# Optimization experiments

Measured on AMD Instinct MI355X. Metric: run time of the kernel, lower is better.

## Reference

```python
import math
import jax, jax.numpy as jnp
import numpy as np

# ---- module hyperparams (from init_kwargs defaults) ----
NUM_AA, EMB_DIM, K, EXCLUDE = 20, 16, 64, 2
R_ON, R_CUT, DELTA, WALL = 8.0, 10.0, 0.3, 10.0
RHO_MIN, RHO_MAX, RHO_BASE = 1.6, 2.8, 2.0
B, L = 8, 2048
BIG = 1e9  # masks excluded pairs in the distance matrix


def setup_inputs() -> dict:
    key = jax.random.key(0)
    k1, k2, k3 = jax.random.split(key, 3)
    # coordinates scaled to a realistic Angstrom spread so switch/softplus are exercised
    R = jax.random.normal(k1, (B, L, 3), dtype=jnp.float32) * 10.0
    seq = jax.random.randint(k2, (B, L), 0, NUM_AA, dtype=jnp.int64)
    # learned params: AA embedding table + size head (small random weight, bias at rho_base)
    emb_table = jax.random.normal(k3, (NUM_AA, EMB_DIM), dtype=jnp.float32)
    size_w = 0.1 * jax.random.normal(jax.random.fold_in(key, 7), (1, EMB_DIM), dtype=jnp.float32)
    frac = (RHO_BASE - RHO_MIN) / max(1e-6, RHO_MAX - RHO_MIN)
    frac = min(0.999, max(0.001, frac))
    size_b = jnp.full((1,), math.log(frac / (1.0 - frac)), dtype=jnp.float32)
    return {"R": R, "seq": seq, "emb_table": emb_table, "size_w": size_w, "size_b": size_b}


def _rho(s, emb_table, size_w, size_b):
    # per-residue learned radius in [RHO_MIN, RHO_MAX]; s: int indices, any shape
    e = emb_table[s]                                  # (..., EMB_DIM)
    x = jnp.einsum('...d,d->...', e, size_w[0]) + size_b[0]
    return RHO_MIN + (RHO_MAX - RHO_MIN) * jax.nn.sigmoid(x)


def _smooth_switch(r):
    # smoothstep from 1 (r<=R_ON) down to 0 (r>=R_CUT)
    t = jnp.clip((r - R_ON) / (R_CUT - R_ON), 0.0, 1.0)
    return 1.0 - t * t * (3.0 - 2.0 * t)


def reference(R, seq, emb_table, size_w, size_b):
    b, l, _ = R.shape
    # pairwise distances (B, L, L)
    diff = R[:, :, None, :] - R[:, None, :, :]
    D = jnp.sqrt(jnp.maximum(jnp.sum(diff * diff, axis=-1), 1e-12))
    # exclude bonded/near-diagonal pairs |i-j| <= EXCLUDE (includes self)
    idx = jnp.arange(l)
    excl = jnp.abs(idx[:, None] - idx[None, :]) <= EXCLUDE
    Dm = jnp.where(excl[None], BIG, D)
    # K smallest distances per residue -> negate for lax.top_k
    neg_r, j = jax.lax.top_k(-Dm, K)                  # (B, L, K)
    r = -neg_r
    # gather neighbor sequence ids along L
    seq_j = jnp.take_along_axis(jnp.broadcast_to(seq[:, :, None], (b, l, K)), j, axis=1)
    # pair radius r0_ij = rho(s_i) + rho(s_j)
    rho_i = _rho(seq, emb_table, size_w, size_b)[:, :, None]   # (B, L, 1)
    rho_j = _rho(seq_j, emb_table, size_w, size_b)             # (B, L, K)
    r0 = rho_i + rho_j
    rep = WALL * jax.nn.softplus((r0 - r) / (DELTA + 1e-12))
    return (rep * _smooth_switch(r)).sum(axis=(1, 2))          # (B,)
```

## Files before the change

### kernel.cpp

```cpp
#include <hip/hip_runtime.h>
#include <hip/hip_fp16.h>
#include <math.h>

#define LRES 2048
#define NB 8
#define KSEL 64
#define EMBD 16
#define NAA 20
#define NBIN 128
#define BINSCALE 1.28f
#define BINW 0.78125f

static __device__ __forceinline__ float fdot2u(unsigned a, unsigned b, float c) {
#if __has_builtin(__builtin_amdgcn_fdot2)
    typedef _Float16 h2f __attribute__((ext_vector_type(2)));
    union { unsigned u; h2f h; } ua, ub;
    ua.u = a; ub.u = b;
    return __builtin_amdgcn_fdot2(ua.h, ub.h, c, false);
#else
    float d;
    asm("v_dot2_f32_f16 %0, %1, %2, %3" : "=v"(d) : "v"(a), "v"(b), "v"(c));
    return d;
#endif
}

static __device__ __forceinline__ unsigned hadd2u(unsigned a, unsigned b) {
    __half2 ha = *(__half2*)&a, hb = *(__half2*)&b;
    __half2 r = __hadd2(ha, hb);
    return *(unsigned*)&r;
}

template <int CTRL, int RM>
static __device__ __forceinline__ unsigned dpp_u(unsigned v) {
    return (unsigned)__builtin_amdgcn_update_dpp(0, (int)v, CTRL, RM, 0xf, true);
}
static __device__ __forceinline__ unsigned wave_iscan_u(unsigned s) {
    s += dpp_u<0x111, 0xf>(s);
    s += dpp_u<0x112, 0xf>(s);
    s += dpp_u<0x114, 0xf>(s);
    s += dpp_u<0x118, 0xf>(s);
    s += dpp_u<0x142, 0xa>(s);
    s += dpp_u<0x143, 0xc>(s);
    return s;
}
static __device__ __forceinline__ float wave_iscan_f(float a) {
    a += __uint_as_float(dpp_u<0x111, 0xf>(__float_as_uint(a)));
    a += __uint_as_float(dpp_u<0x112, 0xf>(__float_as_uint(a)));
    a += __uint_as_float(dpp_u<0x114, 0xf>(__float_as_uint(a)));
    a += __uint_as_float(dpp_u<0x118, 0xf>(__float_as_uint(a)));
    a += __uint_as_float(dpp_u<0x142, 0xa>(__float_as_uint(a)));
    a += __uint_as_float(dpp_u<0x143, 0xc>(__float_as_uint(a)));
    return a;
}

#define LDS_FENCE() asm volatile("s_waitcnt lgkmcnt(0)" ::: "memory")

__global__ __launch_bounds__(512, 8) void repel_kernel(
    const float* __restrict__ R,
    const int* __restrict__ seq,
    const float* __restrict__ emb,
    const float* __restrict__ wv,
    const float* __restrict__ bias,
    float* __restrict__ partial)
{
    const int tid  = threadIdx.x;
    const int w    = tid >> 6;
    const int lane = tid & 63;
    const int row  = blockIdx.x * 8 + w;
    const int b    = row >> 11;
    const int i    = row & (LRES - 1);

    __shared__ uint2    Pl[LRES];
    __shared__ unsigned hist[8][NBIN];
    __shared__ float    rho_tab[NAA];
    __shared__ unsigned shT[8];
    __shared__ float    shS[8];

    const float* __restrict__ Rb = R + b * (LRES * 3);
    const int*   __restrict__ Sb = seq + b * LRES;

    if (tid < NAA) {
        float x = bias[0];
#pragma unroll
        for (int d = 0; d < EMBD; ++d) x += emb[tid * EMBD + d] * wv[d];
        rho_tab[tid] = 1.6f + 1.2f / (1.0f + __expf(-x));
    }
    __syncthreads();

#pragma unroll
    for (int q = 0; q < 4; ++q) {
        int p = (q << 9) + tid;
        float x = Rb[p * 3 + 0], y = Rb[p * 3 + 1], z = Rb[p * 3 + 2];
        float rho = rho_tab[Sb[p]];
        __half2 h0 = __floats2half2_rn(x, y);
        __half2 h1 = __floats2half2_rn(z, rho);
        Pl[p] = make_uint2(*(unsigned*)&h0, *(unsigned*)&h1);
    }

    *(uint2*)&hist[w][lane << 1] = make_uint2(0u, 0u);
    if (lane == 0) shT[w] = NBIN - 1;
    __syncthreads();

    const uint2 ci = Pl[i];
    const unsigned ncxy = ci.x ^ 0x80008000u;
    const unsigned nczv = (ci.y & 0x0000FFFFu) ^ 0x00008000u;
    const float rho_i = __high2float(*(__half2*)&ci.y);

    const int s_i = __builtin_amdgcn_readfirstlane(i);
    const int tlo = ((s_i - 2 > 0) ? (s_i - 2) : 0) >> 7;
    const int thi = ((s_i + 2 < LRES - 1) ? (s_i + 2) : (LRES - 1)) >> 7;

    const unsigned lane2 = (unsigned)lane << 1;
    const unsigned exbits = __float_as_uint(1.0e9f);

    const uint4* __restrict__ P4 = (const uint4*)Pl;
    unsigned d2u[32];
#pragma unroll
    for (int t = 0; t < 16; ++t) {
        uint4 u = P4[(t << 6) + lane];
        int j0 = (t << 7) + (int)lane2;
        unsigned dxyA = hadd2u(u.x, ncxy);
        unsigned dzA  = hadd2u(u.y, nczv) & 0x0000FFFFu;
        float d2a = fdot2u(dxyA, dxyA, fdot2u(dzA, dzA, 0.0f));
        unsigned dxyB = hadd2u(u.z, ncxy);
        unsigned dzB  = hadd2u(u.w, nczv) & 0x0000FFFFu;
        float d2b = fdot2u(dxyB, dxyB, fdot2u(dzB, dzB, 0.0f));
        unsigned dua = __float_as_uint(d2a);
        unsigned dub = __float_as_uint(d2b);
        if (t == tlo || t == thi) {
            int e0 = j0 - i;     e0 = (e0 < 0) ? -e0 : e0;
            int e1 = j0 + 1 - i; e1 = (e1 < 0) ? -e1 : e1;
            if (e0 <= 2) dua = exbits;
            if (e1 <= 2) dub = exbits;
        }
        d2u[2 * t]     = dua;
        d2u[2 * t + 1] = dub;
        if (dua <= 0x42C7FFFFu)
            atomicAdd(&hist[w][(unsigned)(d2a * BINSCALE)], 1u);
        if (dub <= 0x42C7FFFFu)
            atomicAdd(&hist[w][(unsigned)(d2b * BINSCALE)], 1u);
    }
    LDS_FENCE();

    uint2 hv = *(const uint2*)&hist[w][lane << 1];
    unsigned p = hv.x + hv.y;
    unsigned s = wave_iscan_u(p);
    unsigned e0s = s - p;
    if (s >= KSEL && e0s < KSEL) {
        unsigned sub = (e0s + hv.x >= KSEL) ? 0u : 1u;
        shT[w] = (lane << 1) + sub;
    }
    LDS_FENCE();
    const unsigned T   = shT[w];
    const unsigned tkb = __float_as_uint((float)(T + 1) * BINW);

    unsigned selmask = 0u;
#pragma unroll
    for (int m = 0; m < 32; ++m)
        selmask |= (d2u[m] < tkb) ? (1u << m) : 0u;

    float acc = 0.0f;
    unsigned msk = selmask;
    while (msk) {
        unsigned m = (unsigned)__builtin_ctz(msk);
        msk &= msk - 1u;
        unsigned j = ((((m >> 1) << 7) | (m & 1)) | lane2);
        uint2 pj = Pl[j];
        unsigned dxy = hadd2u(pj.x, ncxy);
        unsigned dz  = hadd2u(pj.y, nczv) & 0x0000FFFFu;
        float d2 = fdot2u(dxy, dxy, fdot2u(dz, dz, 0.0f));
        float r  = __fsqrt_rn(fmaxf(d2, 1e-12f));
        float rho_j = __high2float(*(__half2*)&pj.y);
        float x = (rho_i + rho_j - r) * (1.0f / 0.3f);
        float sp = fmaxf(x, 0.0f) + __logf(1.0f + __expf(-fabsf(x)));
        float t = fminf(fmaxf((r - 8.0f) * 0.5f, 0.0f), 1.0f);
        float sw = 1.0f - t * t * (3.0f - 2.0f * t);
        acc += 10.0f * sp * sw;
    }

    float atot = wave_iscan_f(acc);
    float wsum = __uint_as_float(__builtin_amdgcn_readlane(__float_as_uint(atot), 63));
    if (lane == 0) shS[w] = wsum;
    __syncthreads();
    if (tid == 0) {
        float v = 0.0f;
#pragma unroll
        for (int q = 0; q < 8; ++q) v += shS[q];
        partial[blockIdx.x] = v;
    }
}

__global__ void reduce_kernel(const float* __restrict__ partial, float* __restrict__ out) {
    __shared__ float sh[4];
    const int b = blockIdx.x;
    const int tid = threadIdx.x;
    float acc = partial[(b << 8) + tid];
#pragma unroll
    for (int o = 32; o > 0; o >>= 1) acc += __shfl_down(acc, o, 64);
    if ((tid & 63) == 0) sh[tid >> 6] = acc;
    __syncthreads();
    if (tid == 0) out[b] = sh[0] + sh[1] + sh[2] + sh[3];
}

extern "C" void kernel_launch(void* const* d_in, const int* in_sizes, int n_in,
                              void* d_out, int out_size, void* d_ws, size_t ws_size,
                              hipStream_t stream) {
    const float* R    = (const float*)d_in[0];
    const int*   seq  = (const int*)d_in[1];
    const float* emb  = (const float*)d_in[2];
    const float* w    = (const float*)d_in[3];
    const float* bias = (const float*)d_in[4];
    float* out = (float*)d_out;

    float* partial = (float*)d_ws;

    repel_kernel<<<NB * LRES / 8, 512, 0, stream>>>(R, seq, emb, w, bias, partial);
    reduce_kernel<<<NB, 256, 0, stream>>>(partial, out);
}
```

Measured before the change: 81.49 us.

## Process two query rows per wave, sharing LDS loads and packing distances to fp16

Each wave now handles two adjacent residues, so every LDS read of the packed coordinate table serves two distance computations, and the grid shrinks to half as many blocks. The per-block staging of the whole chain into LDS is amortised over 16 rows instead of 8. Squared distances for the two rows are packed as fp16 pairs to keep the register count at 32, and the bin threshold is converted to an fp16 bit pattern for comparison. The costs are more histogram atomics per wave, a serial selection loop over both rows, and fp16 rounding of distances near the selection threshold.

```diff
diff --git a/kernel.cpp b/kernel.cpp
--- a/kernel.cpp
+++ b/kernel.cpp
@@ -30,6 +30,19 @@
     return *(unsigned*)&r;
 }
 
+static __device__ __forceinline__ unsigned pk16(float a, float b) {
+#if __has_builtin(__builtin_amdgcn_cvt_pkrtz)
+    __typeof__(__builtin_amdgcn_cvt_pkrtz(0.0f, 0.0f)) r =
+        __builtin_amdgcn_cvt_pkrtz(a, b);
+    union { __typeof__(r) h; unsigned u; } cv;
+    cv.h = r;
+    return cv.u;
+#else
+    __half2 r = __floats2half2_rn(a, b);
+    return *(unsigned*)&r;
+#endif
+}
+
 template <int CTRL, int RM>
 static __device__ __forceinline__ unsigned dpp_u(unsigned v) {
     return (unsigned)__builtin_amdgcn_update_dpp(0, (int)v, CTRL, RM, 0xf, true);
@@ -66,14 +79,15 @@
     const int tid  = threadIdx.x;
     const int w    = tid >> 6;
     const int lane = tid & 63;
-    const int row  = blockIdx.x * 8 + w;
-    const int b    = row >> 11;
-    const int i    = row & (LRES - 1);
+    const int k    = blockIdx.x;
+    const int b    = k >> 7;
+    const int iA   = ((k & 127) << 4) + (w << 1);
+    const int iB   = iA + 1;
 
     __shared__ uint2    Pl[LRES];
-    __shared__ unsigned hist[8][NBIN];
+    __shared__ unsigned hist[16][NBIN];
     __shared__ float    rho_tab[NAA];
-    __shared__ unsigned shT[8];
+    __shared__ unsigned shT[16];
     __shared__ float    shS[8];
 
     const float* __restrict__ Rb = R + b * (LRES * 3);
@@ -97,85 +111,112 @@
         Pl[p] = make_uint2(*(unsigned*)&h0, *(unsigned*)&h1);
     }
 
-    *(uint2*)&hist[w][lane << 1] = make_uint2(0u, 0u);
-    if (lane == 0) shT[w] = NBIN - 1;
-    __syncthreads();
-
-    const uint2 ci = Pl[i];
-    const unsigned ncxy = ci.x ^ 0x80008000u;
-    const unsigned nczv = (ci.y & 0x0000FFFFu) ^ 0x00008000u;
-    const float rho_i = __high2float(*(__half2*)&ci.y);
-
-    const int s_i = __builtin_amdgcn_readfirstlane(i);
-    const int tlo = ((s_i - 2 > 0) ? (s_i - 2) : 0) >> 7;
-    const int thi = ((s_i + 2 < LRES - 1) ? (s_i + 2) : (LRES - 1)) >> 7;
+    *(uint2*)&hist[(w << 1) + 0][lane << 1] = make_uint2(0u, 0u);
+    *(uint2*)&hist[(w << 1) + 1][lane << 1] = make_uint2(0u, 0u);
+    if (lane == 0) { shT[(w << 1)] = NBIN - 1; shT[(w << 1) + 1] = NBIN - 1; }
+    __syncthreads();
+
+    const uint2 cA = Pl[iA];
+    const unsigned ncxyA = cA.x ^ 0x80008000u;
+    const unsigned nczvA = (cA.y & 0x0000FFFFu) ^ 0x00008000u;
+    const float rho_iA = __high2float(*(__half2*)&cA.y);
+    const uint2 cB = Pl[iB];
+    const unsigned ncxyB = cB.x ^ 0x80008000u;
+    const unsigned nczvB = (cB.y & 0x0000FFFFu) ^ 0x00008000u;
+    const float rho_iB = __high2float(*(__half2*)&cB.y);
+
+    const int s_iA = __builtin_amdgcn_readfirstlane(iA);
+    const int tlo = ((s_iA - 2 > 0) ? (s_iA - 2) : 0) >> 7;
+    const int thi = ((s_iA + 3 < LRES - 1) ? (s_iA + 3) : (LRES - 1)) >> 7;
 
     const unsigned lane2 = (unsigned)lane << 1;
-    const unsigned exbits = __float_as_uint(1.0e9f);
 
     const uint4* __restrict__ P4 = (const uint4*)Pl;
-    unsigned d2u[32];
+    unsigned d2h[32];
 #pragma unroll
     for (int t = 0; t < 16; ++t) {
         uint4 u = P4[(t << 6) + lane];
         int j0 = (t << 7) + (int)lane2;
-        unsigned dxyA = hadd2u(u.x, ncxy);
-        unsigned dzA  = hadd2u(u.y, nczv) & 0x0000FFFFu;
-        float d2a = fdot2u(dxyA, dxyA, fdot2u(dzA, dzA, 0.0f));
-        unsigned dxyB = hadd2u(u.z, ncxy);
-        unsigned dzB  = hadd2u(u.w, nczv) & 0x0000FFFFu;
-        float d2b = fdot2u(dxyB, dxyB, fdot2u(dzB, dzB, 0.0f));
-        unsigned dua = __float_as_uint(d2a);
-        unsigned dub = __float_as_uint(d2b);
+        unsigned dxy, dz;
+        dxy = hadd2u(u.x, ncxyA); dz = hadd2u(u.y, nczvA) & 0x0000FFFFu;
+        float d0A = fdot2u(dxy, dxy, fdot2u(dz, dz, 0.0f));
+        dxy = hadd2u(u.x, ncxyB); dz = hadd2u(u.y, nczvB) & 0x0000FFFFu;
+        float d0B = fdot2u(dxy, dxy, fdot2u(dz, dz, 0.0f));
+        dxy = hadd2u(u.z, ncxyA); dz = hadd2u(u.w, nczvA) & 0x0000FFFFu;
+        float d1A = fdot2u(dxy, dxy, fdot2u(dz, dz, 0.0f));
+        dxy = hadd2u(u.z, ncxyB); dz = hadd2u(u.w, nczvB) & 0x0000FFFFu;
+        float d1B = fdot2u(dxy, dxy, fdot2u(dz, dz, 0.0f));
         if (t == tlo || t == thi) {
-            int e0 = j0 - i;     e0 = (e0 < 0) ? -e0 : e0;
-            int e1 = j0 + 1 - i; e1 = (e1 < 0) ? -e1 : e1;
-            if (e0 <= 2) dua = exbits;
-            if (e1 <= 2) dub = exbits;
+            int e;
+            e = j0 - iA;     e = (e < 0) ? -e : e; if (e <= 2) d0A = 1.0e9f;
+            e = j0 - iB;     e = (e < 0) ? -e : e; if (e <= 2) d0B = 1.0e9f;
+            e = j0 + 1 - iA; e = (e < 0) ? -e : e; if (e <= 2) d1A = 1.0e9f;
+            e = j0 + 1 - iB; e = (e < 0) ? -e : e; if (e <= 2) d1B = 1.0e9f;
         }
-        d2u[2 * t]     = dua;
-        d2u[2 * t + 1] = dub;
-        if (dua <= 0x42C7FFFFu)
-            atomicAdd(&hist[w][(unsigned)(d2a * BINSCALE)], 1u);
-        if (dub <= 0x42C7FFFFu)
-            atomicAdd(&hist[w][(unsigned)(d2b * BINSCALE)], 1u);
+        if (d0A < 100.0f) atomicAdd(&hist[(w << 1) + 0][(unsigned)(d0A * BINSCALE)], 1u);
+        if (d0B < 100.0f) atomicAdd(&hist[(w << 1) + 1][(unsigned)(d0B * BINSCALE)], 1u);
+        if (d1A < 100.0f) atomicAdd(&hist[(w << 1) + 0][(unsigned)(d1A * BINSCALE)], 1u);
+        if (d1B < 100.0f) atomicAdd(&hist[(w << 1) + 1][(unsigned)(d1B * BINSCALE)], 1u);
+        d2h[2 * t]     = pk16(d0A, d0B);
+        d2h[2 * t + 1] = pk16(d1A, d1B);
     }
     LDS_FENCE();
 
-    uint2 hv = *(const uint2*)&hist[w][lane << 1];
-    unsigned p = hv.x + hv.y;
-    unsigned s = wave_iscan_u(p);
-    unsigned e0s = s - p;
-    if (s >= KSEL && e0s < KSEL) {
-        unsigned sub = (e0s + hv.x >= KSEL) ? 0u : 1u;
-        shT[w] = (lane << 1) + sub;
+    uint2 hvA = *(const uint2*)&hist[(w << 1) + 0][lane << 1];
+    uint2 hvB = *(const uint2*)&hist[(w << 1) + 1][lane << 1];
+    unsigned pA = hvA.x + hvA.y, pB = hvB.x + hvB.y;
+    unsigned sA = wave_iscan_u(pA), sB = wave_iscan_u(pB);
+    unsigned eA = sA - pA, eB = sB - pB;
+    if (sA >= KSEL && eA < KSEL) {
+        unsigned sub = (eA + hvA.x >= KSEL) ? 0u : 1u;
+        shT[(w << 1) + 0] = (lane << 1) + sub;
+    }
+    if (sB >= KSEL && eB < KSEL) {
+        unsigned sub = (eB + hvB.x >= KSEL) ? 0u : 1u;
+        shT[(w << 1) + 1] = (lane << 1) + sub;
     }
     LDS_FENCE();
-    const unsigned T   = shT[w];
-    const unsigned tkb = __float_as_uint((float)(T + 1) * BINW);
-
-    unsigned selmask = 0u;
-#pragma unroll
-    for (int m = 0; m < 32; ++m)
-        selmask |= (d2u[m] < tkb) ? (1u << m) : 0u;
+    const unsigned TA = shT[(w << 1) + 0];
+    const unsigned TB = shT[(w << 1) + 1];
+
+    float EAf = (float)(TA + 1) * BINW;
+    __half hA = __float2half_rz(EAf);
+    unsigned thA = (unsigned)__half_as_ushort(hA) + ((__half2float(hA) < EAf) ? 1u : 0u);
+    float EBf = (float)(TB + 1) * BINW;
+    __half hB = __float2half_rz(EBf);
+    unsigned thB = (unsigned)__half_as_ushort(hB) + ((__half2float(hB) < EBf) ? 1u : 0u);
+
+    unsigned selA = 0u, selB = 0u;
+#pragma unroll
+    for (int m = 0; m < 32; ++m) {
+        unsigned v = d2h[m];
+        selA |= ((v & 0xFFFFu) < thA) ? (1u << m) : 0u;
+        selB |= ((v >> 16)     < thB) ? (1u << m) : 0u;
+    }
 
     float acc = 0.0f;
-    unsigned msk = selmask;
-    while (msk) {
-        unsigned m = (unsigned)__builtin_ctz(msk);
-        msk &= msk - 1u;
-        unsigned j = ((((m >> 1) << 7) | (m & 1)) | lane2);
-        uint2 pj = Pl[j];
-        unsigned dxy = hadd2u(pj.x, ncxy);
-        unsigned dz  = hadd2u(pj.y, nczv) & 0x0000FFFFu;
-        float d2 = fdot2u(dxy, dxy, fdot2u(dz, dz, 0.0f));
-        float r  = __fsqrt_rn(fmaxf(d2, 1e-12f));
-        float rho_j = __high2float(*(__half2*)&pj.y);
-        float x = (rho_i + rho_j - r) * (1.0f / 0.3f);
-        float sp = fmaxf(x, 0.0f) + __logf(1.0f + __expf(-fabsf(x)));
-        float t = fminf(fmaxf((r - 8.0f) * 0.5f, 0.0f), 1.0f);
-        float sw = 1.0f - t * t * (3.0f - 2.0f * t);
-        acc += 10.0f * sp * sw;
+#pragma unroll 1
+    for (int rsel = 0; rsel < 2; ++rsel) {
+        unsigned msk      = rsel ? selB : selA;
+        const unsigned nx = rsel ? ncxyB : ncxyA;
+        const unsigned nz = rsel ? nczvB : nczvA;
+        const float    ri = rsel ? rho_iB : rho_iA;
+        while (msk) {
+            unsigned m = (unsigned)__builtin_ctz(msk);
+            msk &= msk - 1u;
+            unsigned j = ((((m >> 1) << 7) | (m & 1)) | lane2);
+            uint2 pj = Pl[j];
+            unsigned dxy = hadd2u(pj.x, nx);
+            unsigned dz  = hadd2u(pj.y, nz) & 0x0000FFFFu;
+            float d2 = fdot2u(dxy, dxy, fdot2u(dz, dz, 0.0f));
+            float r  = __fsqrt_rn(fmaxf(d2, 1e-12f));
+            float rho_j = __high2float(*(__half2*)&pj.y);
+            float x = (ri + rho_j - r) * (1.0f / 0.3f);
+            float sp = fmaxf(x, 0.0f) + __logf(1.0f + __expf(-fabsf(x)));
+            float t = fminf(fmaxf((r - 8.0f) * 0.5f, 0.0f), 1.0f);
+            float sw = 1.0f - t * t * (3.0f - 2.0f * t);
+            acc += 10.0f * sp * sw;
+        }
     }
 
     float atot = wave_iscan_f(acc);
@@ -186,7 +227,7 @@
         float v = 0.0f;
 #pragma unroll
         for (int q = 0; q < 8; ++q) v += shS[q];
-        partial[blockIdx.x] = v;
+        partial[k] = v;
     }
 }
 
@@ -194,7 +235,7 @@
     __shared__ float sh[4];
     const int b = blockIdx.x;
     const int tid = threadIdx.x;
-    float acc = partial[(b << 8) + tid];
+    float acc = (tid < 128) ? partial[(b << 7) + tid] : 0.0f;
 #pragma unroll
     for (int o = 32; o > 0; o >>= 1) acc += __shfl_down(acc, o, 64);
     if ((tid & 63) == 0) sh[tid >> 6] = acc;
@@ -214,6 +255,6 @@
 
     float* partial = (float*)d_ws;
 
-    repel_kernel<<<NB * LRES / 8, 512, 0, stream>>>(R, seq, emb, w, bias, partial);
+    repel_kernel<<<NB * LRES / 16, 512, 0, stream>>>(R, seq, emb, w, bias, partial);
     reduce_kernel<<<NB, 256, 0, stream>>>(partial, out);
 }
```

Result: slower. 94.63 us (+16.1%).
